# Performance work log

Hardware: AMD Instinct MI355X
Metric: run time of the kernel (lower is better)

Reference implementation:

```python
import jax, jax.numpy as jnp
import numpy as np

B, Z, A, H = 2048, 64, 8, 512

def setup_inputs() -> dict:
    key = jax.random.key(0)
    ks = jax.random.split(key, 7)
    s = 1.0 / np.sqrt(H).astype(np.float32)
    z = jax.random.normal(ks[0], (B, Z), jnp.float32)
    # PyTorch LSTM params, gate order [i, f, g, o]
    W_ih = jax.random.uniform(ks[1], (4 * H, A + Z), jnp.float32, -s, s)
    W_hh = jax.random.uniform(ks[2], (4 * H, H), jnp.float32, -s, s)
    b_ih = jax.random.uniform(ks[3], (4 * H,), jnp.float32, -s, s)
    b_hh = jax.random.uniform(ks[4], (4 * H,), jnp.float32, -s, s)
    W_out = jax.random.uniform(ks[5], (A, H), jnp.float32, -s, s)
    b_out = jax.random.uniform(ks[6], (A,), jnp.float32, -s, s)
    return {"z": z, "W_ih": W_ih, "W_hh": W_hh, "b_ih": b_ih, "b_hh": b_hh,
            "W_out": W_out, "b_out": b_out, "seq_len": 64}


def reference(z, W_ih, W_hh, b_ih, b_hh, W_out, b_out, seq_len):
    batch = z.shape[0]
    hidden = W_hh.shape[1]
    act = W_out.shape[0]
    # dec_in_t = [zeros_a, z] is identical at every timestep -> hoist input proj
    dec_in = jnp.concatenate([jnp.zeros((batch, act), z.dtype), z], axis=-1)
    x_proj = dec_in @ W_ih.T + b_ih + b_hh  # (B, 4H), constant per step

    def step(carry, _):
        h, c = carry
        gates = x_proj + h @ W_hh.T  # (B, 4H)
        i, f, g, o = jnp.split(gates, 4, axis=-1)
        i = jax.nn.sigmoid(i)
        f = jax.nn.sigmoid(f)
        g = jnp.tanh(g)
        o = jax.nn.sigmoid(o)
        c = f * c + i * g
        h = o * jnp.tanh(c)
        return (h, c), h

    init = (jnp.zeros((batch, hidden), z.dtype), jnp.zeros((batch, hidden), z.dtype))
    _, hs = jax.lax.scan(step, init, None, length=seq_len)  # (T, B, H)
    hs = jnp.transpose(hs, (1, 0, 2))  # (B, T, H)
    return hs @ W_out.T + b_out  # (B, T, A)
```

## Files before the change

### kernel.cpp

```cpp
#include <hip/hip_runtime.h>


#define HID   512
#define TSTEP 64
#define KCAT  576

typedef __attribute__((ext_vector_type(8))) short bf16x8;
typedef __attribute__((ext_vector_type(4))) float f32x4;

__device__ inline unsigned short f2bf(float f) {
  unsigned int u = __builtin_bit_cast(unsigned int, f);
  unsigned int r = (u + 0x7fffu + ((u >> 16) & 1u)) >> 16;
  return (unsigned short)r;
}
__device__ inline float sigm(float x) { return 1.0f / (1.0f + __expf(-x)); }
__device__ inline float tanh_f(float x) { return 1.0f - 2.0f / (__expf(2.0f * x) + 1.0f); }

__device__ inline void gl16(const unsigned short* g, unsigned short* l) {
  __builtin_amdgcn_global_load_lds(
      (const __attribute__((address_space(1))) unsigned int*)g,
      (__attribute__((address_space(3))) unsigned int*)l, 16, 0, 0);
}

__global__ void k_prep(const float* __restrict__ z, const float* __restrict__ wih,
                       const float* __restrict__ whh, const float* __restrict__ bih,
                       const float* __restrict__ bhh, const float* __restrict__ wout,
                       unsigned short* __restrict__ wcat, unsigned short* __restrict__ zbf,
                       float* __restrict__ bias, unsigned short* __restrict__ wob) {
  int c = blockIdx.x * 256 + threadIdx.x;
  if (c < 147456) {
    int n = c / 72, kc = (c % 72) * 8;
    unsigned short u[8];
#pragma unroll
    for (int e = 0; e < 8; ++e) {
      int k = kc + e;
      float v = (k < 512) ? whh[(size_t)n * 512 + k] : wih[(size_t)n * 72 + 8 + (k - 512)];
      u[e] = f2bf(v);
    }
    *(bf16x8*)&wcat[(size_t)n * KCAT + kc] = *(bf16x8*)u;
  } else if (c < 163840) {
    int i = c - 147456;
    int row = i >> 3, kc = (i & 7) * 8;
    unsigned short u[8];
#pragma unroll
    for (int e = 0; e < 8; ++e) u[e] = f2bf(z[(size_t)row * 64 + kc + e]);
    *(bf16x8*)&zbf[(size_t)row * 64 + kc] = *(bf16x8*)u;
  } else if (c < 165888) {
    int n = c - 163840;
    bias[n] = bih[n] + bhh[n];
  } else if (c < 166912) {
    int i = c - 165888;
    int r = i >> 6, kc = (i & 63) * 8;
    unsigned short u[8];
#pragma unroll
    for (int e = 0; e < 8; ++e) u[e] = (r < 8) ? f2bf(wout[(size_t)r * 512 + kc + e]) : (unsigned short)0;
    *(bf16x8*)&wob[(size_t)r * 512 + kc] = *(bf16x8*)u;
  }
}

template <int GATES, int PROJ>
__global__ __launch_bounds__(256, 2) void k_step(
    const unsigned short* __restrict__ hprev, unsigned short* __restrict__ hnext,
    const unsigned short* __restrict__ wcat, const unsigned short* __restrict__ zbf,
    const unsigned short* __restrict__ wob, const float* __restrict__ bias,
    const float* __restrict__ bout, float* __restrict__ cst,
    float* __restrict__ out, int t) {
  __shared__ unsigned short Ab[2][64 * 64];
  __shared__ unsigned short Bb[2][144 * 64];
  __shared__ unsigned short hO[64 * 40];

  const int bid = blockIdx.x;
  const int nt = GATES ? (((bid & 7) << 1) | ((bid >> 8) & 1)) : 0;
  const int bt = GATES ? ((bid >> 3) & 31) : bid;
  const int tid = threadIdx.x;
  const int lane = tid & 63;
  const int wv = tid >> 6;
  const int mq = wv >> 1, nh = wv & 1;
  const int cl = lane & 15, q8 = lane >> 4;
  const int b0 = bt * 64, j0 = nt * 32;

  const int rA = tid >> 3;
  const int xA = ((tid & 7) ^ (rA & 7)) * 8;
  const unsigned short* srcA0 = hprev + (size_t)(b0 + rA) * HID + xA;
  const unsigned short* srcA1 = hprev + (size_t)(b0 + 32 + rA) * HID + xA;
  const unsigned short* srcZ0 = zbf + (size_t)(b0 + rA) * 64 + xA;
  const unsigned short* srcZ1 = zbf + (size_t)(b0 + 32 + rA) * 64 + xA;
  const unsigned short* srcB[4];
#pragma unroll
  for (int k = 0; k < 4; ++k) {
    int rB = k * 32 + rA;
    int n = (rB >> 5) * HID + j0 + (rB & 31);
    srcB[k] = wcat + (size_t)n * KCAT + xA;
  }
  const unsigned short* srcW = wob + (size_t)(tid >> 3) * HID + xA;

#define STAGE_H(BUF, KK) do { \
    gl16(srcA0 + (KK) * 64, &Ab[BUF][(wv * 64) * 8]); \
    gl16(srcA1 + (KK) * 64, &Ab[BUF][(256 + wv * 64) * 8]); \
    if (GATES) { _Pragma("unroll") for (int k = 0; k < 4; ++k) \
      gl16(srcB[k] + (KK) * 64, &Bb[BUF][(k * 256 + wv * 64) * 8]); } \
    if (PROJ && tid < 128) gl16(srcW + (KK) * 64, &Bb[BUF][(1024 + wv * 64) * 8]); \
  } while (0)
#define STAGE_Z(BUF) do { \
    gl16(srcZ0, &Ab[BUF][(wv * 64) * 8]); \
    gl16(srcZ1, &Ab[BUF][(256 + wv * 64) * 8]); \
    _Pragma("unroll") for (int k = 0; k < 4; ++k) \
      gl16(srcB[k] + 8 * 64, &Bb[BUF][(k * 256 + wv * 64) * 8]); \
  } while (0)

  f32x4 acc[4][2];
  if (GATES) {
#pragma unroll
    for (int g = 0; g < 4; ++g) {
      float bv = bias[g * HID + j0 + nh * 16 + cl];
      f32x4 v = {bv, bv, bv, bv};
      acc[g][0] = v; acc[g][1] = v;
    }
  }
  f32x4 accp0 = {0, 0, 0, 0}, accp1 = {0, 0, 0, 0};
  if (PROJ) {
    float bo = (cl < 8) ? bout[cl] : 0.0f;
    f32x4 v = {bo, bo, bo, bo};
    accp0 = v; accp1 = v;
  }

  const int kkEnd = GATES ? 8 : 7;
  const int kk0 = (GATES && t == 0) ? 8 : 0;
  if (kk0 == 8) STAGE_Z(0); else STAGE_H(0, 0);
  __syncthreads();

  int bu = 0;
  for (int kk = kk0; kk <= kkEnd; ++kk) {
    if (kk < kkEnd) {
      if (kk + 1 == 8) STAGE_Z(bu ^ 1); else STAGE_H(bu ^ 1, kk + 1);
    }
    const unsigned short* Al = Ab[bu];
    const unsigned short* Bl = Bb[bu];
#pragma unroll
    for (int ks = 0; ks < 2; ++ks) {
      const int sx = ((ks * 4 + q8) ^ (cl & 7)) * 8;
      bf16x8 af0 = *(const bf16x8*)&Al[(mq * 32 + cl) * 64 + sx];
      bf16x8 af1 = *(const bf16x8*)&Al[(mq * 32 + 16 + cl) * 64 + sx];
      if (GATES) {
#pragma unroll
        for (int g = 0; g < 4; ++g) {
          bf16x8 bf = *(const bf16x8*)&Bl[(g * 32 + nh * 16 + cl) * 64 + sx];
          acc[g][0] = __builtin_amdgcn_mfma_f32_16x16x32_bf16(af0, bf, acc[g][0], 0, 0, 0);
          acc[g][1] = __builtin_amdgcn_mfma_f32_16x16x32_bf16(af1, bf, acc[g][1], 0, 0, 0);
        }
      }
      if (PROJ && nh == 0 && kk < 8) {
        bf16x8 wf = *(const bf16x8*)&Bl[(128 + cl) * 64 + sx];
        accp0 = __builtin_amdgcn_mfma_f32_16x16x32_bf16(af0, wf, accp0, 0, 0, 0);
        accp1 = __builtin_amdgcn_mfma_f32_16x16x32_bf16(af1, wf, accp1, 0, 0, 0);
      }
    }
    __syncthreads();
    bu ^= 1;
  }

  if (PROJ && nh == 0 && cl < 8) {
    const int tt = t - 1;
#pragma unroll
    for (int r = 0; r < 4; ++r) {
      int b = b0 + mq * 32 + q8 * 4 + r;
      out[((size_t)b * 64 + tt) * 8 + cl] = accp0[r];
      out[((size_t)(b + 16) * 64 + tt) * 8 + cl] = accp1[r];
    }
  }

  if (GATES) {
    const size_t cbase = ((size_t)bid * 256 + tid) * 8;
    f32x4 c0 = {0, 0, 0, 0}, c1 = {0, 0, 0, 0};
    if (t > 0) { c0 = *(const f32x4*)&cst[cbase]; c1 = *(const f32x4*)&cst[cbase + 4]; }
#pragma unroll
    for (int fm = 0; fm < 2; ++fm) {
      f32x4 cold = fm ? c1 : c0;
      f32x4 cn;
#pragma unroll
      for (int r = 0; r < 4; ++r) {
        float iv = sigm(acc[0][fm][r]);
        float fv = sigm(acc[1][fm][r]);
        float gv = tanh_f(acc[2][fm][r]);
        float ov = sigm(acc[3][fm][r]);
        float cv = fv * cold[r] + iv * gv;
        cn[r] = cv;
        hO[(mq * 32 + fm * 16 + q8 * 4 + r) * 40 + nh * 16 + cl] = f2bf(ov * tanh_f(cv));
      }
      if (fm) c1 = cn; else c0 = cn;
    }
    *(f32x4*)&cst[cbase] = c0;
    *(f32x4*)&cst[cbase + 4] = c1;
    __syncthreads();

    int row = tid >> 2, sg4 = tid & 3;
    unsigned short tmp[8];
#pragma unroll
    for (int e = 0; e < 8; ++e) tmp[e] = hO[row * 40 + sg4 * 8 + e];
    *(int4*)&hnext[(size_t)(b0 + row) * HID + j0 + sg4 * 8] = *(int4*)tmp;
  }
#undef STAGE_H
#undef STAGE_Z
}

extern "C" void kernel_launch(void* const* d_in, const int* in_sizes, int n_in,
                              void* d_out, int out_size, void* d_ws, size_t ws_size,
                              hipStream_t stream) {
  const float* z    = (const float*)d_in[0];
  const float* wih  = (const float*)d_in[1];
  const float* whh  = (const float*)d_in[2];
  const float* bih  = (const float*)d_in[3];
  const float* bhh  = (const float*)d_in[4];
  const float* wout = (const float*)d_in[5];
  const float* bout = (const float*)d_in[6];
  float* out = (float*)d_out;

  char* ws = (char*)d_ws;
  unsigned short* wcat = (unsigned short*)(ws);
  unsigned short* zbf  = (unsigned short*)(ws + 2359296);
  float* bias          = (float*)(ws + 2621440);
  unsigned short* wob  = (unsigned short*)(ws + 2629632);
  unsigned short* h0   = (unsigned short*)(ws + 2646016);
  unsigned short* h1   = (unsigned short*)(ws + 4743168);
  float* cst           = (float*)(ws + 6840320);

  k_prep<<<dim3(652), dim3(256), 0, stream>>>(z, wih, whh, bih, bhh, wout,
                                              wcat, zbf, bias, wob);

  for (int t = 0; t < TSTEP; ++t) {
    const unsigned short* hp = (t & 1) ? h0 : h1;
    unsigned short* hn = (t & 1) ? h1 : h0;
    if (t == 0)
      k_step<1, 0><<<dim3(512), dim3(256), 0, stream>>>(hp, hn, wcat, zbf, wob, bias,
                                                        bout, cst, out, t);
    else
      k_step<1, 1><<<dim3(512), dim3(256), 0, stream>>>(hp, hn, wcat, zbf, wob, bias,
                                                        bout, cst, out, t);
  }
  k_step<0, 1><<<dim3(32), dim3(256), 0, stream>>>(h1, h0, wcat, zbf, wob, bias,
                                                   bout, cst, out, TSTEP);
}
```

Baseline: 946.8 us.

## Deepen LDS pipeline with manual waitcnt barriers and stage W_out in LDS

The K-loop now keeps two stages in flight, using explicit s_waitcnt vmcnt counts and raw s_barrier in place of a __syncthreads after every K chunk. The output projection weights are converted from fp32 to bf16 inside each step kernel and held whole in a swizzled LDS buffer, instead of being streamed per K chunk from a prepacked workspace copy. The cell-state load is hoisted ahead of the GEMM so its latency overlaps the compute. LDS use per block grows by about 16KB, and the hand-counted vmcnt values are fragile if the number of loads issued per stage changes.

```diff
diff --git a/kernel.cpp b/kernel.cpp
--- a/kernel.cpp
+++ b/kernel.cpp
@@ -24,9 +24,9 @@
 
 __global__ void k_prep(const float* __restrict__ z, const float* __restrict__ wih,
                        const float* __restrict__ whh, const float* __restrict__ bih,
-                       const float* __restrict__ bhh, const float* __restrict__ wout,
+                       const float* __restrict__ bhh,
                        unsigned short* __restrict__ wcat, unsigned short* __restrict__ zbf,
-                       float* __restrict__ bias, unsigned short* __restrict__ wob) {
+                       float* __restrict__ bias) {
   int c = blockIdx.x * 256 + threadIdx.x;
   if (c < 147456) {
     int n = c / 72, kc = (c % 72) * 8;
@@ -48,13 +48,6 @@
   } else if (c < 165888) {
     int n = c - 163840;
     bias[n] = bih[n] + bhh[n];
-  } else if (c < 166912) {
-    int i = c - 165888;
-    int r = i >> 6, kc = (i & 63) * 8;
-    unsigned short u[8];
-#pragma unroll
-    for (int e = 0; e < 8; ++e) u[e] = (r < 8) ? f2bf(wout[(size_t)r * 512 + kc + e]) : (unsigned short)0;
-    *(bf16x8*)&wob[(size_t)r * 512 + kc] = *(bf16x8*)u;
   }
 }
 
@@ -62,11 +55,12 @@
 __global__ __launch_bounds__(256, 2) void k_step(
     const unsigned short* __restrict__ hprev, unsigned short* __restrict__ hnext,
     const unsigned short* __restrict__ wcat, const unsigned short* __restrict__ zbf,
-    const unsigned short* __restrict__ wob, const float* __restrict__ bias,
+    const float* __restrict__ wout, const float* __restrict__ bias,
     const float* __restrict__ bout, float* __restrict__ cst,
     float* __restrict__ out, int t) {
   __shared__ unsigned short Ab[2][64 * 64];
-  __shared__ unsigned short Bb[2][144 * 64];
+  __shared__ unsigned short Bb[2][128 * 64];
+  __shared__ unsigned short wo_lds[16 * 512];
   __shared__ unsigned short hO[64 * 40];
 
   const int bid = blockIdx.x;
@@ -92,21 +86,42 @@
     int n = (rB >> 5) * HID + j0 + (rB & 31);
     srcB[k] = wcat + (size_t)n * KCAT + xA;
   }
-  const unsigned short* srcW = wob + (size_t)(tid >> 3) * HID + xA;
-
-#define STAGE_H(BUF, KK) do { \
-    gl16(srcA0 + (KK) * 64, &Ab[BUF][(wv * 64) * 8]); \
-    gl16(srcA1 + (KK) * 64, &Ab[BUF][(256 + wv * 64) * 8]); \
-    if (GATES) { _Pragma("unroll") for (int k = 0; k < 4; ++k) \
-      gl16(srcB[k] + (KK) * 64, &Bb[BUF][(k * 256 + wv * 64) * 8]); } \
-    if (PROJ && tid < 128) gl16(srcW + (KK) * 64, &Bb[BUF][(1024 + wv * 64) * 8]); \
-  } while (0)
-#define STAGE_Z(BUF) do { \
-    gl16(srcZ0, &Ab[BUF][(wv * 64) * 8]); \
-    gl16(srcZ1, &Ab[BUF][(256 + wv * 64) * 8]); \
-    _Pragma("unroll") for (int k = 0; k < 4; ++k) \
-      gl16(srcB[k] + 8 * 64, &Bb[BUF][(k * 256 + wv * 64) * 8]); \
-  } while (0)
+
+  auto do_stage = [&](int buf, int kkv) {
+    if (GATES) {
+      if (kkv == 8) {
+        gl16(srcZ0, &Ab[buf][(wv * 64) * 8]);
+        gl16(srcZ1, &Ab[buf][(256 + wv * 64) * 8]);
+      } else {
+        gl16(srcA0 + kkv * 64, &Ab[buf][(wv * 64) * 8]);
+        gl16(srcA1 + kkv * 64, &Ab[buf][(256 + wv * 64) * 8]);
+      }
+#pragma unroll
+      for (int k = 0; k < 4; ++k)
+        gl16(srcB[k] + kkv * 64, &Bb[buf][(k * 256 + wv * 64) * 8]);
+    } else {
+      gl16(srcA0 + kkv * 64, &Ab[buf][(wv * 64) * 8]);
+      gl16(srcA1 + kkv * 64, &Ab[buf][(256 + wv * 64) * 8]);
+    }
+  };
+
+  if (PROJ) {
+    int r = tid >> 4, s0 = tid & 15;
+#pragma unroll
+    for (int i = 0; i < 4; ++i) {
+      int s = s0 + i * 16;
+      unsigned short u[8] = {0, 0, 0, 0, 0, 0, 0, 0};
+      if (r < 8) {
+        const float* wp = wout + (size_t)r * 512 + s * 8;
+        float4 f0 = *(const float4*)wp;
+        float4 f1 = *(const float4*)(wp + 4);
+        u[0] = f2bf(f0.x); u[1] = f2bf(f0.y); u[2] = f2bf(f0.z); u[3] = f2bf(f0.w);
+        u[4] = f2bf(f1.x); u[5] = f2bf(f1.y); u[6] = f2bf(f1.z); u[7] = f2bf(f1.w);
+      }
+      int off = r * 512 + (s >> 3) * 64 + (((s & 7) ^ (r & 7)) * 8);
+      *(bf16x8*)&wo_lds[off] = *(bf16x8*)u;
+    }
+  }
 
   f32x4 acc[4][2];
   if (GATES) {
@@ -124,16 +139,11 @@
     accp0 = v; accp1 = v;
   }
 
-  const int kkEnd = GATES ? 8 : 7;
-  const int kk0 = (GATES && t == 0) ? 8 : 0;
-  if (kk0 == 8) STAGE_Z(0); else STAGE_H(0, 0);
-  __syncthreads();
-
-  int bu = 0;
-  for (int kk = kk0; kk <= kkEnd; ++kk) {
-    if (kk < kkEnd) {
-      if (kk + 1 == 8) STAGE_Z(bu ^ 1); else STAGE_H(bu ^ 1, kk + 1);
-    }
+  const size_t cbase = ((size_t)bid * 256 + tid) * 8;
+  f32x4 c0 = {0, 0, 0, 0}, c1 = {0, 0, 0, 0};
+  if (GATES && t > 0) { c0 = *(const f32x4*)&cst[cbase]; c1 = *(const f32x4*)&cst[cbase + 4]; }
+
+  auto mfma_block = [&](int bu, int kkv) {
     const unsigned short* Al = Ab[bu];
     const unsigned short* Bl = Bb[bu];
 #pragma unroll
@@ -149,14 +159,42 @@
           acc[g][1] = __builtin_amdgcn_mfma_f32_16x16x32_bf16(af1, bf, acc[g][1], 0, 0, 0);
         }
       }
-      if (PROJ && nh == 0 && kk < 8) {
-        bf16x8 wf = *(const bf16x8*)&Bl[(128 + cl) * 64 + sx];
+      if (PROJ && nh == 0 && kkv < 8) {
+        bf16x8 wf = *(const bf16x8*)&wo_lds[cl * 512 + kkv * 64 + sx];
         accp0 = __builtin_amdgcn_mfma_f32_16x16x32_bf16(af0, wf, accp0, 0, 0, 0);
         accp1 = __builtin_amdgcn_mfma_f32_16x16x32_bf16(af1, wf, accp1, 0, 0, 0);
       }
     }
-    __syncthreads();
-    bu ^= 1;
+  };
+
+#define MEMBAR() asm volatile("" ::: "memory")
+#define HWBAR()  __builtin_amdgcn_s_barrier()
+
+  if (GATES && t == 0) {
+    do_stage(0, 8);
+    asm volatile("s_waitcnt vmcnt(0) lgkmcnt(0)" ::: "memory");
+    HWBAR(); MEMBAR();
+    mfma_block(0, 8);
+  } else {
+    do_stage(0, 0);
+    do_stage(1, 1);
+    if (GATES) asm volatile("s_waitcnt vmcnt(6) lgkmcnt(0)" ::: "memory");
+    else       asm volatile("s_waitcnt vmcnt(2) lgkmcnt(0)" ::: "memory");
+    HWBAR(); MEMBAR();
+    const int kkEnd = GATES ? 8 : 7;
+    for (int kk = 0;; ++kk) {
+      mfma_block(kk & 1, kk);
+      if (kk == kkEnd) break;
+      MEMBAR(); HWBAR(); MEMBAR();
+      if (kk + 2 <= kkEnd) {
+        do_stage(kk & 1, kk + 2);
+        if (GATES) asm volatile("s_waitcnt vmcnt(6)" ::: "memory");
+        else       asm volatile("s_waitcnt vmcnt(2)" ::: "memory");
+      } else {
+        asm volatile("s_waitcnt vmcnt(0)" ::: "memory");
+      }
+      MEMBAR(); HWBAR(); MEMBAR();
+    }
   }
 
   if (PROJ && nh == 0 && cl < 8) {
@@ -170,9 +208,6 @@
   }
 
   if (GATES) {
-    const size_t cbase = ((size_t)bid * 256 + tid) * 8;
-    f32x4 c0 = {0, 0, 0, 0}, c1 = {0, 0, 0, 0};
-    if (t > 0) { c0 = *(const f32x4*)&cst[cbase]; c1 = *(const f32x4*)&cst[cbase + 4]; }
 #pragma unroll
     for (int fm = 0; fm < 2; ++fm) {
       f32x4 cold = fm ? c1 : c0;
@@ -199,8 +234,8 @@
     for (int e = 0; e < 8; ++e) tmp[e] = hO[row * 40 + sg4 * 8 + e];
     *(int4*)&hnext[(size_t)(b0 + row) * HID + j0 + sg4 * 8] = *(int4*)tmp;
   }
-#undef STAGE_H
-#undef STAGE_Z
+#undef MEMBAR
+#undef HWBAR
 }
 
 extern "C" void kernel_launch(void* const* d_in, const int* in_sizes, int n_in,
@@ -219,24 +254,22 @@
   unsigned short* wcat = (unsigned short*)(ws);
   unsigned short* zbf  = (unsigned short*)(ws + 2359296);
   float* bias          = (float*)(ws + 2621440);
-  unsigned short* wob  = (unsigned short*)(ws + 2629632);
-  unsigned short* h0   = (unsigned short*)(ws + 2646016);
-  unsigned short* h1   = (unsigned short*)(ws + 4743168);
-  float* cst           = (float*)(ws + 6840320);
-
-  k_prep<<<dim3(652), dim3(256), 0, stream>>>(z, wih, whh, bih, bhh, wout,
-                                              wcat, zbf, bias, wob);
+  unsigned short* h0   = (unsigned short*)(ws + 2629632);
+  unsigned short* h1   = (unsigned short*)(ws + 4726784);
+  float* cst           = (float*)(ws + 6823936);
+
+  k_prep<<<dim3(648), dim3(256), 0, stream>>>(z, wih, whh, bih, bhh, wcat, zbf, bias);
 
   for (int t = 0; t < TSTEP; ++t) {
     const unsigned short* hp = (t & 1) ? h0 : h1;
     unsigned short* hn = (t & 1) ? h1 : h0;
     if (t == 0)
-      k_step<1, 0><<<dim3(512), dim3(256), 0, stream>>>(hp, hn, wcat, zbf, wob, bias,
+      k_step<1, 0><<<dim3(512), dim3(256), 0, stream>>>(hp, hn, wcat, zbf, wout, bias,
                                                         bout, cst, out, t);
     else
-      k_step<1, 1><<<dim3(512), dim3(256), 0, stream>>>(hp, hn, wcat, zbf, wob, bias,
+      k_step<1, 1><<<dim3(512), dim3(256), 0, stream>>>(hp, hn, wcat, zbf, wout, bias,
                                                         bout, cst, out, t);
   }
-  k_step<0, 1><<<dim3(32), dim3(256), 0, stream>>>(h1, h0, wcat, zbf, wob, bias,
+  k_step<0, 1><<<dim3(32), dim3(256), 0, stream>>>(h1, h0, wcat, zbf, wout, bias,
                                                    bout, cst, out, TSTEP);
 }
```

Result: faster. 926.7 us (-2.1%).
